# Kernel tuning notes

Hardware: AMD Instinct MI355X
Metric: run time of the kernel (lower is better)

## Reference

```python
import jax, jax.numpy as jnp
import numpy as np

B, T, H, NH = 4, 2048, 1024, 16
HD = H // NH  # 64


def setup_inputs() -> dict:
    key = jax.random.key(0)
    ks = jax.random.split(key, 8)
    s = 1.0 / np.sqrt(H)
    return {
        "hidden_states": jax.random.normal(ks[0], (B, T, H), dtype=jnp.float32),
        "attention_mask": jnp.zeros((B, 1, 1, T), dtype=jnp.float32),
        "Wq": jax.random.normal(ks[1], (H, H), dtype=jnp.float32) * s,
        "bq": jax.random.normal(ks[2], (H,), dtype=jnp.float32) * 0.01,
        "Wk": jax.random.normal(ks[3], (H, H), dtype=jnp.float32) * s,
        "bk": jax.random.normal(ks[4], (H,), dtype=jnp.float32) * 0.01,
        "Wv": jax.random.normal(ks[5], (H, H), dtype=jnp.float32) * s,
        "bv": jax.random.normal(ks[6], (H,), dtype=jnp.float32) * 0.01,
    }


def _split_heads(x):
    # [b, t, h*d] -> [b, h, t, d]
    b, t, _ = x.shape
    return x.reshape(b, t, NH, HD).transpose(0, 2, 1, 3)


def reference(hidden_states, attention_mask, Wq, bq, Wk, bk, Wv, bv):
    q = _split_heads(hidden_states @ Wq.T + bq)
    k = _split_heads(hidden_states @ Wk.T + bk)
    v = _split_heads(hidden_states @ Wv.T + bv)
    scores = jnp.einsum('bhqd,bhkd->bhqk', q, k) / jnp.sqrt(jnp.float32(HD))
    t = q.shape[2]
    causal = jnp.triu(jnp.ones((t, t), dtype=scores.dtype), k=1)[None, None] * (-1e9)
    scores = scores + causal + attention_mask
    probs = jax.nn.softmax(scores, axis=-1)
    # module returns [b, h, t, d] (no merge back)
    return jnp.einsum('bhqk,bhkd->bhqd', probs, v)
```

## Files before the change

### kernel.cpp

```cpp
#include <hip/hip_runtime.h>
#include <hip/hip_bf16.h>


typedef float  f32x4 __attribute__((ext_vector_type(4)));
typedef short  s16x8 __attribute__((ext_vector_type(8)));
typedef unsigned short u16;

#define LOG2E 1.44269504088896340736f

__device__ __forceinline__ u16 f2bf(float f) {
  unsigned u = __float_as_uint(f);
  u += 0x7FFFu + ((u >> 16) & 1u);
  return (u16)(u >> 16);
}

__device__ __forceinline__ float ex2(float x) {
#if __has_builtin(__builtin_amdgcn_exp2f)
  return __builtin_amdgcn_exp2f(x);
#else
  return exp2f(x);
#endif
}
__device__ __forceinline__ float rcp_(float x) {
#if __has_builtin(__builtin_amdgcn_rcpf)
  return __builtin_amdgcn_rcpf(x);
#else
  return 1.0f / x;
#endif
}
__device__ __forceinline__ unsigned cvtpk(float lo, float hi) {
  unsigned r;
  asm("v_cvt_pk_bf16_f32 %0, %1, %2" : "=v"(r) : "v"(lo), "v"(hi));
  return r;
}
__device__ __forceinline__ void bar() {
  asm volatile("" ::: "memory");
  __builtin_amdgcn_s_barrier();
  asm volatile("" ::: "memory");
}

#define GLOAD16(gp, lp)                                                          \
  __builtin_amdgcn_global_load_lds(                                              \
      (const __attribute__((address_space(1))) void*)(gp),                       \
      (__attribute__((address_space(3))) void*)(lp), 16, 0, 0)

#define MFMA(a, b, c) __builtin_amdgcn_mfma_f32_16x16x32_bf16((a), (b), (c), 0, 0, 0)

__global__ __launch_bounds__(256) void cvt_all(
    const float* __restrict__ hs, const float* __restrict__ wq,
    const float* __restrict__ wk, const float* __restrict__ wv,
    u16* __restrict__ xo, u16* __restrict__ qo, u16* __restrict__ ko,
    u16* __restrict__ vo) {
  int b = blockIdx.x;
  const float* s;
  u16* d;
  size_t i;
  if (b < 4096) { s = hs; d = xo; i = (size_t)b * 256 + threadIdx.x; }
  else {
    int w = (b - 4096) >> 9, r = (b - 4096) & 511;
    s = (w == 0) ? wq : (w == 1) ? wk : wv;
    d = (w == 0) ? qo : (w == 1) ? ko : vo;
    i = (size_t)r * 256 + threadIdx.x;
  }
  const float4* sp = (const float4*)s + i * 2;
  float4 a = sp[0], c = sp[1];
  s16x8 r8;
  r8[0] = f2bf(a.x); r8[1] = f2bf(a.y); r8[2] = f2bf(a.z); r8[3] = f2bf(a.w);
  r8[4] = f2bf(c.x); r8[5] = f2bf(c.y); r8[6] = f2bf(c.z); r8[7] = f2bf(c.w);
  *(s16x8*)(d + i * 8) = r8;
}

__global__ __launch_bounds__(512, 2) void qkv_gemm(
    const u16* __restrict__ Xb,
    const u16* __restrict__ Wqb, const u16* __restrict__ Wkb,
    const u16* __restrict__ Wvb,
    const float* __restrict__ bq, const float* __restrict__ bk,
    const float* __restrict__ bv,
    u16* __restrict__ Qo, u16* __restrict__ Ko, u16* __restrict__ Vto) {
  int bid0 = blockIdx.x;
  int bid  = (bid0 & 7) * 96 + (bid0 >> 3);
  int which = bid % 3;
  int rt = bid / 3;
  int mt = rt >> 3, nt = rt & 7;
  const u16* W = (which == 0) ? Wqb : (which == 1) ? Wkb : Wvb;
  const float* bias = (which == 0) ? bq : (which == 1) ? bk : bv;

  __shared__ __align__(16) char lds[98304];

  int tid = threadIdx.x;
  int lane = tid & 63, wid = tid >> 6;
  int q16 = lane & 15, g = lane >> 4;
  int wr = wid >> 1, wc = wid & 1;

  int srow = tid >> 3, sslot = tid & 7;
  int sw = (sslot ^ (srow & 7)) << 4;
  const char* Asrc = (const char*)Xb + (size_t)(mt * 256 + srow) * 2048 + sw;
  const char* Bsrc = (const char*)W  + (size_t)(nt * 128 + srow) * 2048 + sw;

  int slot0 = (g ^ (q16 & 7)) << 4;

#define STAGE_AB(tt, buf) do { size_t so = (size_t)(tt) * 128;                   \
    GLOAD16(Asrc + so,          lds + (buf) * 32768 + tid * 16);                 \
    GLOAD16(Asrc + so + 131072, lds + (buf) * 32768 + 8192 + tid * 16);          \
    GLOAD16(Asrc + so + 262144, lds + (buf) * 32768 + 16384 + tid * 16);         \
    GLOAD16(Asrc + so + 393216, lds + (buf) * 32768 + 24576 + tid * 16);         \
    GLOAD16(Bsrc + so,          lds + 65536 + (buf) * 16384 + tid * 16);         \
    GLOAD16(Bsrc + so + 131072, lds + 65536 + (buf) * 16384 + 8192 + tid * 16); } while (0)

#define LDA(FA, buf, mp) do {                                                    \
    const char* p_ = lds + (buf) * 32768 + (wr * 64 + (mp) * 32 + q16) * 128;    \
    FA[0] = *(const s16x8*)(p_ + slot0);                                         \
    FA[1] = *(const s16x8*)(p_ + (slot0 ^ 64));                                  \
    FA[2] = *(const s16x8*)(p_ + 2048 + slot0);                                  \
    FA[3] = *(const s16x8*)(p_ + 2048 + (slot0 ^ 64)); } while (0)

#define LDB(FB, buf) do {                                                        \
    const char* p_ = lds + 65536 + (buf) * 16384 + (wc * 64 + q16) * 128;        \
    FB[0] = *(const s16x8*)(p_ + slot0);                                         \
    FB[1] = *(const s16x8*)(p_ + (slot0 ^ 64));                                  \
    FB[2] = *(const s16x8*)(p_ + 2048 + slot0);                                  \
    FB[3] = *(const s16x8*)(p_ + 2048 + (slot0 ^ 64));                           \
    FB[4] = *(const s16x8*)(p_ + 4096 + slot0);                                  \
    FB[5] = *(const s16x8*)(p_ + 4096 + (slot0 ^ 64));                           \
    FB[6] = *(const s16x8*)(p_ + 6144 + slot0);                                  \
    FB[7] = *(const s16x8*)(p_ + 6144 + (slot0 ^ 64)); } while (0)

#define MM16(mlo, FA, FB) do {                                                   \
    _Pragma("unroll")                                                            \
    for (int n_ = 0; n_ < 4; ++n_) {                                             \
      acc[(mlo)][n_]     = MFMA(FA[0], FB[2 * n_],     acc[(mlo)][n_]);          \
      acc[(mlo)][n_]     = MFMA(FA[1], FB[2 * n_ + 1], acc[(mlo)][n_]);          \
      acc[(mlo) + 1][n_] = MFMA(FA[2], FB[2 * n_],     acc[(mlo) + 1][n_]);      \
      acc[(mlo) + 1][n_] = MFMA(FA[3], FB[2 * n_ + 1], acc[(mlo) + 1][n_]);      \
    } } while (0)

  STAGE_AB(0, 0);

  f32x4 acc[4][4] = {};
  s16x8 fA0[4], fA1[4], fB[8];

#pragma unroll 1
  for (int i = 0; i < 16; ++i) {
    int buf = i & 1;
    if (i < 15) {
      STAGE_AB(i + 1, buf ^ 1);
      asm volatile("s_waitcnt vmcnt(6)" ::: "memory");
    } else {
      asm volatile("s_waitcnt vmcnt(0)" ::: "memory");
    }
    bar();
    LDA(fA0, buf, 0);
    LDA(fA1, buf, 1);
    LDB(fB, buf);
    __builtin_amdgcn_s_setprio(1);
    MM16(0, fA0, fB);
    MM16(2, fA1, fB);
    __builtin_amdgcn_s_setprio(0);
    bar();
  }

  u16* tile = (u16*)(void*)lds + (size_t)wid * 64 * 72;
  int h0 = nt * 2 + wc;
  int m_base = mt * 256 + wr * 64;
  int bb = m_base >> 11;
  int t0 = m_base & 2047;

  if (which != 2) {
    float qsc = (which == 0) ? (0.125f * LOG2E) : 1.0f;
#pragma unroll
    for (int n = 0; n < 4; ++n) {
      float bvl = bias[h0 * 64 + n * 16 + q16];
#pragma unroll
      for (int m = 0; m < 4; ++m)
#pragma unroll
        for (int j = 0; j < 4; ++j)
          tile[(m * 16 + g * 4 + j) * 72 + n * 16 + q16] =
              f2bf((acc[m][n][j] + bvl) * qsc);
    }
  } else {
#pragma unroll
    for (int n = 0; n < 4; ++n) {
      float bvl = bias[h0 * 64 + n * 16 + q16];
#pragma unroll
      for (int m = 0; m < 4; ++m)
#pragma unroll
        for (int j = 0; j < 4; ++j)
          tile[(n * 16 + q16) * 72 + m * 16 + g * 4 + j] =
              f2bf(acc[m][n][j] + bvl);
    }
  }
  asm volatile("" ::: "memory");

  const char* tb = (const char*)tile;
  int rl = lane >> 3, cb = (lane & 7) * 16;
  if (which != 2) {
    u16* Out = (which == 0) ? Qo : Ko;
    char* gbase = (char*)(Out + ((size_t)(bb * 16 + h0) * 2048 + t0) * 64);
#pragma unroll
    for (int c = 0; c < 8; ++c) {
      int row = rl + c * 8;
      s16x8 v = *(const s16x8*)(tb + row * 144 + cb);
      *(s16x8*)(gbase + row * 128 + cb) = v;
    }
  } else {
    char* gbase = (char*)Vto + ((size_t)(bb * 16 + h0) * 64) * 4096 + t0 * 2;
#pragma unroll
    for (int c = 0; c < 8; ++c) {
      int d = rl + c * 8;
      s16x8 v = *(const s16x8*)(tb + d * 144 + cb);
      *(s16x8*)(gbase + (size_t)d * 4096 + cb) = v;
    }
  }
#undef STAGE_AB
#undef LDA
#undef LDB
#undef MM16
}

__global__ __launch_bounds__(256) void attn_fwd(
    const u16* __restrict__ Qw, const u16* __restrict__ Kw,
    const u16* __restrict__ Vtw, const float* __restrict__ maskp,
    float* __restrict__ out) {
  int bid0 = blockIdx.x;
  int bid = (bid0 & 7) * 256 + (bid0 >> 3);
  int bh = bid >> 5, qt = bid & 31;
  int qb = qt << 6;
  int tid = threadIdx.x;
  int lane = tid & 63, wid = tid >> 6;
  int q16 = lane & 15, g = lane >> 4;

  __shared__ __align__(16) char Ks[2][8192];
  __shared__ __align__(16) char Vs[2][8192];
  __shared__ __align__(16) float maskl[2048];

  size_t qrow = (size_t)bh * 2048 + qb + wid * 16 + q16;
  s16x8 qa0 = *(const s16x8*)(Qw + qrow * 64 + g * 8);
  s16x8 qa1 = *(const s16x8*)(Qw + qrow * 64 + 32 + g * 8);

  int srow = tid >> 3;
  int sinner = (tid & 7) << 4;
  int fs = (srow & 7) ^ ((srow >> 1) & 4);
  int ssw = sinner ^ (fs << 4);
  const char* Kg = (const char*)Kw + ((size_t)bh * 2048 + srow) * 128 + ssw;
  const char* Vg = (const char*)Vtw + ((size_t)bh * 64 + srow) * 4096 + ssw;

  {
    const float* mrow = maskp + (size_t)(bh >> 4) * 2048;
    f32x4 a = *(const f32x4*)(mrow + tid * 4);
    f32x4 b = *(const f32x4*)(mrow + 1024 + tid * 4);
    *(f32x4*)(maskl + tid * 4) = a * LOG2E;
    *(f32x4*)(maskl + 1024 + tid * 4) = b * LOG2E;
  }

  GLOAD16(Kg, Ks[0] + tid * 16);
  GLOAD16(Kg + 4096, Ks[0] + tid * 16 + 4096);
  GLOAD16(Vg, Vs[0] + tid * 16);
  GLOAD16(Vg + 131072, Vs[0] + tid * 16 + 4096);
  __syncthreads();

  f32x4 o[4] = {};
  f32x4 lones = {};
  const s16x8 ones = {0x3F80, 0x3F80, 0x3F80, 0x3F80, 0x3F80, 0x3F80, 0x3F80, 0x3F80};

  int qcol = qb + wid * 16 + q16;
  int ntile = qt + 1;

  for (int kt = 0; kt < ntile; ++kt) {
    int cur = kt & 1;
    if (kt + 1 < ntile) {
      size_t kb2 = (size_t)(kt + 1) << 6;
      char* kd = Ks[cur ^ 1] + tid * 16;
      char* vd = Vs[cur ^ 1] + tid * 16;
      GLOAD16(Kg + kb2 * 128, kd);
      GLOAD16(Kg + kb2 * 128 + 4096, kd + 4096);
      GLOAD16(Vg + kb2 * 2, vd);
      GLOAD16(Vg + kb2 * 2 + 131072, vd + 4096);
      asm volatile("s_waitcnt vmcnt(4)" ::: "memory");
    } else {
      asm volatile("s_waitcnt vmcnt(0)" ::: "memory");
    }
    __builtin_amdgcn_s_barrier();
    asm volatile("" ::: "memory");

    int kb = kt << 6;
    const char* ksb = Ks[cur];
    const char* vsb = Vs[cur];
    bool causal = (kt == qt);

#pragma unroll
    for (int c = 0; c < 2; ++c) {
      f32x4 sA[2];
      __builtin_amdgcn_s_setprio(1);
#pragma unroll
      for (int t4 = 0; t4 < 2; ++t4) {
        int kk = 32 * c + ((q16 >> 2) << 3) + (t4 << 2) + (q16 & 3);
        int fk = (kk & 7) ^ ((kk >> 1) & 4);
        const char* krow = ksb + kk * 128;
        int in0 = (g * 16) ^ (fk << 4);
        s16x8 kf0 = *(const s16x8*)(krow + in0);
        s16x8 kf1 = *(const s16x8*)(krow + (in0 ^ 64));
        f32x4 sv = {0.f, 0.f, 0.f, 0.f};
        sv = MFMA(kf0, qa0, sv);
        sv = MFMA(kf1, qa1, sv);
        sA[t4] = sv;
      }
      __builtin_amdgcn_s_setprio(0);

      union { s16x8 v; unsigned u[4]; } pb;
#pragma unroll
      for (int t4 = 0; t4 < 2; ++t4) {
        f32x4 mv = *(const f32x4*)(maskl + kb + 32 * c + 8 * g + 4 * t4);
        float p0 = ex2(sA[t4][0] + mv[0]);
        float p1 = ex2(sA[t4][1] + mv[1]);
        float p2 = ex2(sA[t4][2] + mv[2]);
        float p3 = ex2(sA[t4][3] + mv[3]);
        if (causal) {
          int k0 = kb + 32 * c + 8 * g + 4 * t4;
          p0 = (k0 + 0 <= qcol) ? p0 : 0.f;
          p1 = (k0 + 1 <= qcol) ? p1 : 0.f;
          p2 = (k0 + 2 <= qcol) ? p2 : 0.f;
          p3 = (k0 + 3 <= qcol) ? p3 : 0.f;
        }
        pb.u[t4 * 2 + 0] = cvtpk(p0, p1);
        pb.u[t4 * 2 + 1] = cvtpk(p2, p3);
      }

      __builtin_amdgcn_s_setprio(1);
#pragma unroll
      for (int dt = 0; dt < 4; ++dt) {
        int d = dt * 16 + q16;
        int fv = (d & 7) ^ ((d >> 1) & 4);
        s16x8 vf = *(const s16x8*)(vsb + d * 128 + ((64 * c + 16 * g) ^ (fv << 4)));
        o[dt] = MFMA(vf, pb.v, o[dt]);
      }
      lones = MFMA(ones, pb.v, lones);
      __builtin_amdgcn_s_setprio(0);
    }
    __builtin_amdgcn_s_barrier();
  }

  float inv = rcp_(lones[0]);
  float* orow = out + ((size_t)bh * 2048 + qb + wid * 16 + q16) * 64 + g * 4;
#pragma unroll
  for (int dt = 0; dt < 4; ++dt)
    *(f32x4*)(orow + dt * 16) = o[dt] * inv;
}

extern "C" void kernel_launch(void* const* d_in, const int* in_sizes, int n_in,
                              void* d_out, int out_size, void* d_ws, size_t ws_size,
                              hipStream_t stream) {
  const float* hs   = (const float*)d_in[0];
  const float* mask = (const float*)d_in[1];
  const float* Wq   = (const float*)d_in[2];
  const float* bq   = (const float*)d_in[3];
  const float* Wk   = (const float*)d_in[4];
  const float* bk   = (const float*)d_in[5];
  const float* Wv   = (const float*)d_in[6];
  const float* bv   = (const float*)d_in[7];
  float* out = (float*)d_out;

  char* w = (char*)d_ws;
  u16* Xb  = (u16*)w; w += (size_t)8192 * 1024 * 2;
  u16* Wqb = (u16*)w; w += (size_t)1024 * 1024 * 2;
  u16* Wkb = (u16*)w; w += (size_t)1024 * 1024 * 2;
  u16* Wvb = (u16*)w; w += (size_t)1024 * 1024 * 2;
  u16* Qw  = (u16*)w; w += (size_t)8192 * 1024 * 2;
  u16* Kw  = (u16*)w; w += (size_t)8192 * 1024 * 2;
  u16* Vtw = (u16*)w; w += (size_t)8192 * 1024 * 2;

  cvt_all<<<5632, 256, 0, stream>>>(hs, Wq, Wk, Wv, Xb, Wqb, Wkb, Wvb);
  qkv_gemm<<<768, 512, 0, stream>>>(Xb, Wqb, Wkb, Wvb, bq, bk, bv, Qw, Kw, Vtw);
  attn_fwd<<<2048, 256, 0, stream>>>(Qw, Kw, Vtw, mask, out);
}
```

Before: 146.8 us.

## Double query rows per wave and fold mask into V as multiplicative weights

Each attention block now covers 128 query rows, with each wave handling two 16-row query fragments, so every K/V tile staged in LDS feeds twice as many MFMAs and half as many blocks are launched. The additive mask is turned into a multiplicative bf16 weight exp(mask), computed in the conversion kernel, multiplied into V in the GEMM epilogue, and used as the row-sum operand in place of a ones vector. This removes the per-element mask add from the softmax inner loop and shrinks the LDS mask buffer. In exchange it doubles accumulator register pressure, coarsens the causal load balance, and loses bf16 precision and dynamic range for large mask values, since exp(-1e9) underflows to zero.

```diff
diff --git a/kernel.cpp b/kernel.cpp
--- a/kernel.cpp
+++ b/kernel.cpp
@@ -13,7 +13,9 @@
   u += 0x7FFFu + ((u >> 16) & 1u);
   return (u16)(u >> 16);
 }
-
+__device__ __forceinline__ float bf2f(u16 v) {
+  return __uint_as_float(((unsigned)v) << 16);
+}
 __device__ __forceinline__ float ex2(float x) {
 #if __has_builtin(__builtin_amdgcn_exp2f)
   return __builtin_amdgcn_exp2f(x);
@@ -49,24 +51,36 @@
 __global__ __launch_bounds__(256) void cvt_all(
     const float* __restrict__ hs, const float* __restrict__ wq,
     const float* __restrict__ wk, const float* __restrict__ wv,
+    const float* __restrict__ maskp,
     u16* __restrict__ xo, u16* __restrict__ qo, u16* __restrict__ ko,
-    u16* __restrict__ vo) {
+    u16* __restrict__ vo, u16* __restrict__ wm) {
   int b = blockIdx.x;
   const float* s;
   u16* d;
   size_t i;
+  bool isw = false;
   if (b < 4096) { s = hs; d = xo; i = (size_t)b * 256 + threadIdx.x; }
-  else {
+  else if (b < 5632) {
     int w = (b - 4096) >> 9, r = (b - 4096) & 511;
     s = (w == 0) ? wq : (w == 1) ? wk : wv;
     d = (w == 0) ? qo : (w == 1) ? ko : vo;
     i = (size_t)r * 256 + threadIdx.x;
+  } else {
+    s = maskp; d = wm; i = (size_t)(b - 5632) * 256 + threadIdx.x;
+    isw = true;
   }
   const float4* sp = (const float4*)s + i * 2;
   float4 a = sp[0], c = sp[1];
   s16x8 r8;
-  r8[0] = f2bf(a.x); r8[1] = f2bf(a.y); r8[2] = f2bf(a.z); r8[3] = f2bf(a.w);
-  r8[4] = f2bf(c.x); r8[5] = f2bf(c.y); r8[6] = f2bf(c.z); r8[7] = f2bf(c.w);
+  if (isw) {
+    r8[0] = f2bf(ex2(a.x * LOG2E)); r8[1] = f2bf(ex2(a.y * LOG2E));
+    r8[2] = f2bf(ex2(a.z * LOG2E)); r8[3] = f2bf(ex2(a.w * LOG2E));
+    r8[4] = f2bf(ex2(c.x * LOG2E)); r8[5] = f2bf(ex2(c.y * LOG2E));
+    r8[6] = f2bf(ex2(c.z * LOG2E)); r8[7] = f2bf(ex2(c.w * LOG2E));
+  } else {
+    r8[0] = f2bf(a.x); r8[1] = f2bf(a.y); r8[2] = f2bf(a.z); r8[3] = f2bf(a.w);
+    r8[4] = f2bf(c.x); r8[5] = f2bf(c.y); r8[6] = f2bf(c.z); r8[7] = f2bf(c.w);
+  }
   *(s16x8*)(d + i * 8) = r8;
 }
 
@@ -75,7 +89,7 @@
     const u16* __restrict__ Wqb, const u16* __restrict__ Wkb,
     const u16* __restrict__ Wvb,
     const float* __restrict__ bq, const float* __restrict__ bk,
-    const float* __restrict__ bv,
+    const float* __restrict__ bv, const u16* __restrict__ Wm,
     u16* __restrict__ Qo, u16* __restrict__ Ko, u16* __restrict__ Vto) {
   int bid0 = blockIdx.x;
   int bid  = (bid0 & 7) * 96 + (bid0 >> 3);
@@ -178,6 +192,13 @@
               f2bf((acc[m][n][j] + bvl) * qsc);
     }
   } else {
+    const u16* wrow = Wm + (size_t)bb * 2048 + t0;
+    float wv[4][4];
+#pragma unroll
+    for (int m = 0; m < 4; ++m)
+#pragma unroll
+      for (int j = 0; j < 4; ++j)
+        wv[m][j] = bf2f(wrow[m * 16 + g * 4 + j]);
 #pragma unroll
     for (int n = 0; n < 4; ++n) {
       float bvl = bias[h0 * 64 + n * 16 + q16];
@@ -186,7 +207,7 @@
 #pragma unroll
         for (int j = 0; j < 4; ++j)
           tile[(n * 16 + q16) * 72 + m * 16 + g * 4 + j] =
-              f2bf(acc[m][n][j] + bvl);
+              f2bf((acc[m][n][j] + bvl) * wv[m][j]);
     }
   }
   asm volatile("" ::: "memory");
@@ -217,25 +238,28 @@
 #undef MM16
 }
 
-__global__ __launch_bounds__(256) void attn_fwd(
+__global__ __launch_bounds__(256, 4) void attn_fwd(
     const u16* __restrict__ Qw, const u16* __restrict__ Kw,
-    const u16* __restrict__ Vtw, const float* __restrict__ maskp,
+    const u16* __restrict__ Vtw, const u16* __restrict__ Wm,
     float* __restrict__ out) {
   int bid0 = blockIdx.x;
-  int bid = (bid0 & 7) * 256 + (bid0 >> 3);
-  int bh = bid >> 5, qt = bid & 31;
-  int qb = qt << 6;
+  int bid = (bid0 & 7) * 128 + (bid0 >> 3);
+  int bh = bid >> 4, qt = bid & 15;
+  int qb = qt << 7;
   int tid = threadIdx.x;
   int lane = tid & 63, wid = tid >> 6;
   int q16 = lane & 15, g = lane >> 4;
 
   __shared__ __align__(16) char Ks[2][8192];
   __shared__ __align__(16) char Vs[2][8192];
-  __shared__ __align__(16) float maskl[2048];
-
-  size_t qrow = (size_t)bh * 2048 + qb + wid * 16 + q16;
-  s16x8 qa0 = *(const s16x8*)(Qw + qrow * 64 + g * 8);
-  s16x8 qa1 = *(const s16x8*)(Qw + qrow * 64 + 32 + g * 8);
+  __shared__ __align__(16) u16 wl[2048];
+
+  int qw0 = qb + wid * 32;
+  size_t qr = (size_t)bh * 2048 + qw0 + q16;
+  s16x8 qa00 = *(const s16x8*)(Qw + qr * 64 + g * 8);
+  s16x8 qa01 = *(const s16x8*)(Qw + qr * 64 + 32 + g * 8);
+  s16x8 qa10 = *(const s16x8*)(Qw + (qr + 16) * 64 + g * 8);
+  s16x8 qa11 = *(const s16x8*)(Qw + (qr + 16) * 64 + 32 + g * 8);
 
   int srow = tid >> 3;
   int sinner = (tid & 7) << 4;
@@ -244,26 +268,19 @@
   const char* Kg = (const char*)Kw + ((size_t)bh * 2048 + srow) * 128 + ssw;
   const char* Vg = (const char*)Vtw + ((size_t)bh * 64 + srow) * 4096 + ssw;
 
-  {
-    const float* mrow = maskp + (size_t)(bh >> 4) * 2048;
-    f32x4 a = *(const f32x4*)(mrow + tid * 4);
-    f32x4 b = *(const f32x4*)(mrow + 1024 + tid * 4);
-    *(f32x4*)(maskl + tid * 4) = a * LOG2E;
-    *(f32x4*)(maskl + 1024 + tid * 4) = b * LOG2E;
-  }
-
+  GLOAD16((const char*)Wm + (size_t)(bh >> 4) * 4096 + tid * 16,
+          (char*)wl + tid * 16);
   GLOAD16(Kg, Ks[0] + tid * 16);
   GLOAD16(Kg + 4096, Ks[0] + tid * 16 + 4096);
   GLOAD16(Vg, Vs[0] + tid * 16);
   GLOAD16(Vg + 131072, Vs[0] + tid * 16 + 4096);
   __syncthreads();
 
-  f32x4 o[4] = {};
-  f32x4 lones = {};
-  const s16x8 ones = {0x3F80, 0x3F80, 0x3F80, 0x3F80, 0x3F80, 0x3F80, 0x3F80, 0x3F80};
-
-  int qcol = qb + wid * 16 + q16;
-  int ntile = qt + 1;
+  f32x4 o0[4] = {}, o1[4] = {};
+  f32x4 lw0 = {}, lw1 = {};
+
+  int qc0 = qw0 + q16, qc1 = qc0 + 16;
+  int ntile = 2 * qt + 2;
 
   for (int kt = 0; kt < ntile; ++kt) {
     int cur = kt & 1;
@@ -285,65 +302,83 @@
     int kb = kt << 6;
     const char* ksb = Ks[cur];
     const char* vsb = Vs[cur];
-    bool causal = (kt == qt);
-
-#pragma unroll
-    for (int c = 0; c < 2; ++c) {
-      f32x4 sA[2];
-      __builtin_amdgcn_s_setprio(1);
-#pragma unroll
-      for (int t4 = 0; t4 < 2; ++t4) {
-        int kk = 32 * c + ((q16 >> 2) << 3) + (t4 << 2) + (q16 & 3);
-        int fk = (kk & 7) ^ ((kk >> 1) & 4);
-        const char* krow = ksb + kk * 128;
-        int in0 = (g * 16) ^ (fk << 4);
-        s16x8 kf0 = *(const s16x8*)(krow + in0);
-        s16x8 kf1 = *(const s16x8*)(krow + (in0 ^ 64));
-        f32x4 sv = {0.f, 0.f, 0.f, 0.f};
-        sv = MFMA(kf0, qa0, sv);
-        sv = MFMA(kf1, qa1, sv);
-        sA[t4] = sv;
+
+    if (64 * kt <= qw0 + 31) {
+      bool causal = (64 * kt + 63 > qw0);
+#pragma unroll
+      for (int c = 0; c < 2; ++c) {
+        f32x4 sA0[2], sA1[2];
+        __builtin_amdgcn_s_setprio(1);
+#pragma unroll
+        for (int t4 = 0; t4 < 2; ++t4) {
+          int kk = 32 * c + ((q16 >> 2) << 3) + (t4 << 2) + (q16 & 3);
+          int fk = (kk & 7) ^ ((kk >> 1) & 4);
+          const char* krow = ksb + kk * 128;
+          int in0 = (g * 16) ^ (fk << 4);
+          s16x8 kf0 = *(const s16x8*)(krow + in0);
+          s16x8 kf1 = *(const s16x8*)(krow + (in0 ^ 64));
+          f32x4 sv = {0.f, 0.f, 0.f, 0.f};
+          sv = MFMA(kf0, qa00, sv);
+          sv = MFMA(kf1, qa01, sv);
+          sA0[t4] = sv;
+          f32x4 su = {0.f, 0.f, 0.f, 0.f};
+          su = MFMA(kf0, qa10, su);
+          su = MFMA(kf1, qa11, su);
+          sA1[t4] = su;
+        }
+        __builtin_amdgcn_s_setprio(0);
+
+        s16x8 wf = *(const s16x8*)((const char*)wl + (kb + 32 * c + 8 * g) * 2);
+
+        union { s16x8 v; unsigned u[4]; } pb0, pb1;
+#pragma unroll
+        for (int t4 = 0; t4 < 2; ++t4) {
+          float a0 = ex2(sA0[t4][0]), a1 = ex2(sA0[t4][1]);
+          float a2 = ex2(sA0[t4][2]), a3 = ex2(sA0[t4][3]);
+          float b0 = ex2(sA1[t4][0]), b1 = ex2(sA1[t4][1]);
+          float b2 = ex2(sA1[t4][2]), b3 = ex2(sA1[t4][3]);
+          if (causal) {
+            int k0 = kb + 32 * c + 8 * g + 4 * t4;
+            a0 = (k0 + 0 <= qc0) ? a0 : 0.f;
+            a1 = (k0 + 1 <= qc0) ? a1 : 0.f;
+            a2 = (k0 + 2 <= qc0) ? a2 : 0.f;
+            a3 = (k0 + 3 <= qc0) ? a3 : 0.f;
+            b0 = (k0 + 0 <= qc1) ? b0 : 0.f;
+            b1 = (k0 + 1 <= qc1) ? b1 : 0.f;
+            b2 = (k0 + 2 <= qc1) ? b2 : 0.f;
+            b3 = (k0 + 3 <= qc1) ? b3 : 0.f;
+          }
+          pb0.u[t4 * 2 + 0] = cvtpk(a0, a1);
+          pb0.u[t4 * 2 + 1] = cvtpk(a2, a3);
+          pb1.u[t4 * 2 + 0] = cvtpk(b0, b1);
+          pb1.u[t4 * 2 + 1] = cvtpk(b2, b3);
+        }
+
+        __builtin_amdgcn_s_setprio(1);
+#pragma unroll
+        for (int dt = 0; dt < 4; ++dt) {
+          int d = dt * 16 + q16;
+          int fv = (d & 7) ^ ((d >> 1) & 4);
+          s16x8 vf = *(const s16x8*)(vsb + d * 128 + ((64 * c + 16 * g) ^ (fv << 4)));
+          o0[dt] = MFMA(vf, pb0.v, o0[dt]);
+          o1[dt] = MFMA(vf, pb1.v, o1[dt]);
+        }
+        lw0 = MFMA(wf, pb0.v, lw0);
+        lw1 = MFMA(wf, pb1.v, lw1);
+        __builtin_amdgcn_s_setprio(0);
       }
-      __builtin_amdgcn_s_setprio(0);
-
-      union { s16x8 v; unsigned u[4]; } pb;
-#pragma unroll
-      for (int t4 = 0; t4 < 2; ++t4) {
-        f32x4 mv = *(const f32x4*)(maskl + kb + 32 * c + 8 * g + 4 * t4);
-        float p0 = ex2(sA[t4][0] + mv[0]);
-        float p1 = ex2(sA[t4][1] + mv[1]);
-        float p2 = ex2(sA[t4][2] + mv[2]);
-        float p3 = ex2(sA[t4][3] + mv[3]);
-        if (causal) {
-          int k0 = kb + 32 * c + 8 * g + 4 * t4;
-          p0 = (k0 + 0 <= qcol) ? p0 : 0.f;
-          p1 = (k0 + 1 <= qcol) ? p1 : 0.f;
-          p2 = (k0 + 2 <= qcol) ? p2 : 0.f;
-          p3 = (k0 + 3 <= qcol) ? p3 : 0.f;
-        }
-        pb.u[t4 * 2 + 0] = cvtpk(p0, p1);
-        pb.u[t4 * 2 + 1] = cvtpk(p2, p3);
-      }
-
-      __builtin_amdgcn_s_setprio(1);
-#pragma unroll
-      for (int dt = 0; dt < 4; ++dt) {
-        int d = dt * 16 + q16;
-        int fv = (d & 7) ^ ((d >> 1) & 4);
-        s16x8 vf = *(const s16x8*)(vsb + d * 128 + ((64 * c + 16 * g) ^ (fv << 4)));
-        o[dt] = MFMA(vf, pb.v, o[dt]);
-      }
-      lones = MFMA(ones, pb.v, lones);
-      __builtin_amdgcn_s_setprio(0);
     }
     __builtin_amdgcn_s_barrier();
   }
 
-  float inv = rcp_(lones[0]);
-  float* orow = out + ((size_t)bh * 2048 + qb + wid * 16 + q16) * 64 + g * 4;
-#pragma unroll
-  for (int dt = 0; dt < 4; ++dt)
-    *(f32x4*)(orow + dt * 16) = o[dt] * inv;
+  float i0 = rcp_(lw0[0]), i1 = rcp_(lw1[0]);
+  float* op0 = out + ((size_t)bh * 2048 + qc0) * 64 + g * 4;
+  float* op1 = out + ((size_t)bh * 2048 + qc1) * 64 + g * 4;
+#pragma unroll
+  for (int dt = 0; dt < 4; ++dt) {
+    *(f32x4*)(op0 + dt * 16) = o0[dt] * i0;
+    *(f32x4*)(op1 + dt * 16) = o1[dt] * i1;
+  }
 }
 
 extern "C" void kernel_launch(void* const* d_in, const int* in_sizes, int n_in,
@@ -367,8 +402,9 @@
   u16* Qw  = (u16*)w; w += (size_t)8192 * 1024 * 2;
   u16* Kw  = (u16*)w; w += (size_t)8192 * 1024 * 2;
   u16* Vtw = (u16*)w; w += (size_t)8192 * 1024 * 2;
-
-  cvt_all<<<5632, 256, 0, stream>>>(hs, Wq, Wk, Wv, Xb, Wqb, Wkb, Wvb);
-  qkv_gemm<<<768, 512, 0, stream>>>(Xb, Wqb, Wkb, Wvb, bq, bk, bv, Qw, Kw, Vtw);
-  attn_fwd<<<2048, 256, 0, stream>>>(Qw, Kw, Vtw, mask, out);
-}
+  u16* Wm  = (u16*)w; w += (size_t)8192 * 2;
+
+  cvt_all<<<5636, 256, 0, stream>>>(hs, Wq, Wk, Wv, mask, Xb, Wqb, Wkb, Wvb, Wm);
+  qkv_gemm<<<768, 512, 0, stream>>>(Xb, Wqb, Wkb, Wvb, bq, bk, bv, Wm, Qw, Kw, Vtw);
+  attn_fwd<<<1024, 256, 0, stream>>>(Qw, Kw, Vtw, Wm, out);
+}
```

New measurement: 142.0 us. 1.03x faster.
